# Kernel tuning notes

Hardware: AMD Instinct MI355X
Metric: run time of the kernel (lower is better)

The kernel has to match this reference:

```python
import jax, jax.numpy as jnp
import numpy as np

BANDWIDTH = 8.0  # gaussian kernel std


def setup_inputs() -> dict:
    key = jax.random.key(0)
    k1, k2 = jax.random.split(key)
    B, N, M, D = 2, 8192, 8192, 64
    return {
        "points": jax.random.normal(k1, (B, N, D), dtype=jnp.float32),
        "ref_points": jax.random.normal(k2, (B, M, D), dtype=jnp.float32),
    }


def reference(points, ref_points):
    # Squared pairwise distances via the |x|^2 + |y|^2 - 2<x,y> expansion
    # (same math as ((x_i - y_j)**2).sum(-1), avoids a [B,N,M,D] intermediate).
    sq_p = jnp.sum(points * points, axis=-1)          # [B,N]
    sq_r = jnp.sum(ref_points * ref_points, axis=-1)  # [B,M]
    s_ij = (sq_p[:, :, None] + sq_r[:, None, :]
            - 2.0 * jnp.einsum('bnd,bmd->bnm', points, ref_points))  # [B,N,M]
    # Gaussian kernel
    k_ij = jnp.exp(s_ij * (-1.0 / (2.0 * BANDWIDTH ** 2)))  # [B,N,M]
    # Weighted mean of reference points (nominator.sum(2) / k_ij.sum(2))
    nominator = jnp.einsum('bnm,bmd->bnd', k_ij, ref_points)  # [B,N,D]
    denominator = jnp.sum(k_ij, axis=-1, keepdims=True)       # [B,N,1]
    return nominator / denominator
```

## Files before the change

### kernel.cpp

```cpp
#include <hip/hip_runtime.h>

constexpr int B_ = 2, N_ = 8192, M_ = 8192, Dd = 64;
constexpr int TN = 128;
constexpr int TM = 64;
constexpr int SPLIT = 8;
constexpr int MCHUNK = M_ / SPLIT;
constexpr int NCHUNKS = MCHUNK / TM;
constexpr int NT = N_ / TN;
constexpr float LOG2E   = 1.4426950408889634f;
constexpr float SCALE_S = LOG2E / 64.0f;
constexpr float SCALE_N = -LOG2E / 128.0f;

using s16x8 = __attribute__((ext_vector_type(8))) short;
using f32x4 = __attribute__((ext_vector_type(4))) float;
using f32x2v = __attribute__((ext_vector_type(2))) float;
using bf16x2 = __attribute__((ext_vector_type(2))) __bf16;

#if defined(__has_builtin)
#if __has_builtin(__builtin_amdgcn_exp2f)
#define EXP2(x) __builtin_amdgcn_exp2f(x)
#endif
#endif
#ifndef EXP2
#define EXP2(x) exp2f(x)
#endif

__device__ __forceinline__ unsigned pk2(float lo, float hi) {
  f32x2v f;
  f[0] = lo;
  f[1] = hi;
  bf16x2 h = __builtin_convertvector(f, bf16x2);
  return __builtin_bit_cast(unsigned, h);
}
__device__ __forceinline__ f32x4 mfma16(s16x8 a, s16x8 b, f32x4 c) {
  return __builtin_amdgcn_mfma_f32_16x16x32_bf16(a, b, c, 0, 0, 0);
}


__global__ __launch_bounds__(256, 4) void msflash_kernel(
    const float* __restrict__ pts, const float* __restrict__ ref,
    float* __restrict__ num_acc, float* __restrict__ den_acc) {
  __shared__ unsigned short ldsY [TM][72];
  __shared__ unsigned short ldsYT[Dd][64];
  __shared__ unsigned short ldsP [4][32][72];
  __shared__ float lds_an2[TN];
  __shared__ float lds_bm2[TM];

  const int tid  = threadIdx.x;
  const int w    = tid >> 6;
  const int lane = tid & 63;
  const int l15  = lane & 15, quad = lane >> 4;
  const int ytsw = quad + (l15 & 7);

  const int s  = blockIdx.x & (SPLIT - 1);
  const int r  = blockIdx.x >> 3;
  const int bb = r / NT;
  const int nt = r % NT;
  const int n0 = nt * TN;
  const int m_begin = s * MCHUNK;

  unsigned short (*ldsX)[72] = (unsigned short (*)[72]) & ldsP[0][0][0];
  {
    const int rowl = tid >> 1, half = tid & 1;
    const float* gp = pts + ((size_t)bb * N_ + n0 + rowl) * Dd + half * 32;
    float sq = 0.f;
    unsigned pkd[16];
#pragma unroll
    for (int i = 0; i < 8; i++) {
      float4 f = ((const float4*)gp)[i];
      sq += f.x * f.x + f.y * f.y + f.z * f.z + f.w * f.w;
      pkd[2 * i + 0] = pk2(f.x, f.y);
      pkd[2 * i + 1] = pk2(f.z, f.w);
    }
    sq += __shfl_xor(sq, 1);
    if (half == 0) lds_an2[rowl] = sq * SCALE_N;
    uint4* dv = (uint4*)&ldsX[rowl][half * 32];
#pragma unroll
    for (int i = 0; i < 4; i++)
      dv[i] = make_uint4(pkd[4 * i], pkd[4 * i + 1], pkd[4 * i + 2], pkd[4 * i + 3]);
  }
  __syncthreads();

  s16x8 bx[2][2];
  float anr_s[2];
#pragma unroll
  for (int rt = 0; rt < 2; rt++) {
#pragma unroll
    for (int ks = 0; ks < 2; ks++)
      bx[rt][ks] = *(const s16x8*)&ldsX[w * 32 + rt * 16 + l15][ks * 32 + quad * 8];
    anr_s[rt] = lds_an2[w * 32 + rt * 16 + l15];
  }

  f32x4 o[2][4], den[2];
#pragma unroll
  for (int rt = 0; rt < 2; rt++) {
    den[rt] = f32x4{0.f, 0.f, 0.f, 0.f};
#pragma unroll
    for (int dt = 0; dt < 4; dt++) o[rt][dt] = f32x4{0.f, 0.f, 0.f, 0.f};
  }
  s16x8 ones;
#pragma unroll
  for (int j = 0; j < 8; j++) ones[j] = (l15 == 0) ? (short)0x3F80 : (short)0;

  for (int c = 0; c < NCHUNKS; c++) {
    __syncthreads();
    {
      const int rowl = tid >> 2, q = tid & 3;
      const float* gp = ref + ((size_t)bb * M_ + m_begin + c * TM + rowl) * Dd + q * 16;
      float sq = 0.f;
      unsigned pkd[8];
#pragma unroll
      for (int i = 0; i < 4; i++) {
        float4 f = ((const float4*)gp)[i];
        sq += f.x * f.x + f.y * f.y + f.z * f.z + f.w * f.w;
        pkd[2 * i + 0] = pk2(f.x, f.y);
        pkd[2 * i + 1] = pk2(f.z, f.w);
      }
      sq += __shfl_xor(sq, 1);
      sq += __shfl_xor(sq, 2);
      if (q == 0) lds_bm2[rowl] = sq * SCALE_N;
      uint4* dv = (uint4*)&ldsY[rowl][q * 16];
      dv[0] = make_uint4(pkd[0], pkd[1], pkd[2], pkd[3]);
      dv[1] = make_uint4(pkd[4], pkd[5], pkd[6], pkd[7]);
      const int tsw = (rowl >> 3) + 2 * q;
      const int mlo = rowl & 7;
#pragma unroll
      for (int j = 0; j < 8; j++) {
        const int d0 = q * 16 + 2 * j;
        const int c0 = (tsw + ((2 * j) & 7)) & 7;
        const int c1 = (tsw + ((2 * j + 1) & 7)) & 7;
        ldsYT[d0][(c0 << 3) + mlo]     = (unsigned short)pkd[j];
        ldsYT[d0 + 1][(c1 << 3) + mlo] = (unsigned short)(pkd[j] >> 16);
      }
    }
    __syncthreads();

    f32x4 sf[2][4];
#pragma unroll
    for (int ct = 0; ct < 4; ct++) {
      s16x8 a0 = *(const s16x8*)&ldsY[ct * 16 + l15][quad * 8];
      s16x8 a1 = *(const s16x8*)&ldsY[ct * 16 + l15][32 + quad * 8];
#pragma unroll
      for (int rt = 0; rt < 2; rt++) {
        f32x4 acc = f32x4{0.f, 0.f, 0.f, 0.f};
        acc = mfma16(a0, bx[rt][0], acc);
        acc = mfma16(a1, bx[rt][1], acc);
        sf[rt][ct] = acc;
      }
    }
#pragma unroll
    for (int ct = 0; ct < 4; ct++) {
      f32x4 bm = *(const f32x4*)&lds_bm2[ct * 16 + quad * 4];
#pragma unroll
      for (int rt = 0; rt < 2; rt++) {
        float e0 = EXP2(sf[rt][ct][0] * SCALE_S + (anr_s[rt] + bm[0]));
        float e1 = EXP2(sf[rt][ct][1] * SCALE_S + (anr_s[rt] + bm[1]));
        float e2 = EXP2(sf[rt][ct][2] * SCALE_S + (anr_s[rt] + bm[2]));
        float e3 = EXP2(sf[rt][ct][3] * SCALE_S + (anr_s[rt] + bm[3]));
        uint2 w2 = make_uint2(pk2(e0, e1), pk2(e2, e3));
        *(uint2*)&ldsP[w][rt * 16 + l15][ct * 16 + quad * 4] = w2;
      }
    }
    s16x8 pf[2][2];
#pragma unroll
    for (int rt = 0; rt < 2; rt++)
#pragma unroll
      for (int ks = 0; ks < 2; ks++)
        pf[rt][ks] = *(const s16x8*)&ldsP[w][rt * 16 + l15][ks * 32 + quad * 8];
#pragma unroll
    for (int dt = 0; dt < 4; dt++) {
      const unsigned short* yt = &ldsYT[dt * 16 + l15][0];
      s16x8 a0 = *(const s16x8*)&yt[(((ytsw + 2 * dt) & 7)) << 3];
      s16x8 a1 = *(const s16x8*)&yt[(((ytsw + 4 + 2 * dt) & 7)) << 3];
#pragma unroll
      for (int rt = 0; rt < 2; rt++) {
        o[rt][dt] = mfma16(a0, pf[rt][0], o[rt][dt]);
        o[rt][dt] = mfma16(a1, pf[rt][1], o[rt][dt]);
      }
    }
#pragma unroll
    for (int rt = 0; rt < 2; rt++) {
      den[rt] = mfma16(ones, pf[rt][0], den[rt]);
      den[rt] = mfma16(ones, pf[rt][1], den[rt]);
    }
  }

  float* ldsO = (float*)&ldsP[w][0][0];
  float* nb = num_acc + ((size_t)bb * N_ + n0) * Dd;
#pragma unroll
  for (int rt = 0; rt < 2; rt++) {
#pragma unroll
    for (int dt = 0; dt < 4; dt++) {
      const int base = l15 * 66 + dt * 16 + quad * 4;
      *(float2*)&ldsO[base + 0] = make_float2(o[rt][dt][0], o[rt][dt][1]);
      *(float2*)&ldsO[base + 2] = make_float2(o[rt][dt][2], o[rt][dt][3]);
    }
    const int nrow = w * 32 + rt * 16;
#pragma unroll
    for (int rr = 0; rr < 16; rr++) {
      float v = ldsO[rr * 66 + lane];
      atomicAdd(&nb[(size_t)(nrow + rr) * Dd + lane], v);
    }
    if (quad == 0)
      atomicAdd(&den_acc[(size_t)bb * N_ + n0 + nrow + l15], den[rt][0]);
  }
}

__global__ __launch_bounds__(256) void msdiv_kernel(
    const float* __restrict__ num, const float* __restrict__ den,
    float* __restrict__ out) {
  const int i = blockIdx.x * 256 + threadIdx.x;
  float4 v = ((const float4*)num)[i];
  const float inv = 1.0f / den[i >> 4];
  ((float4*)out)[i] = make_float4(v.x * inv, v.y * inv, v.z * inv, v.w * inv);
}

extern "C" void kernel_launch(void* const* d_in, const int* in_sizes, int n_in,
                              void* d_out, int out_size, void* d_ws, size_t ws_size,
                              hipStream_t stream) {
  const float* pts = (const float*)d_in[0];
  const float* ref = (const float*)d_in[1];
  float* out = (float*)d_out;
  float* num = (float*)d_ws;
  float* den = num + (size_t)B_ * N_ * Dd;
  const size_t acc_bytes = ((size_t)B_ * N_ * Dd + (size_t)B_ * N_) * sizeof(float);

  hipMemsetAsync(d_ws, 0, acc_bytes, stream);
  msflash_kernel<<<dim3(B_ * NT * SPLIT), dim3(256), 0, stream>>>(pts, ref, num, den);
  const int tot4 = B_ * N_ * Dd / 4;
  msdiv_kernel<<<dim3(tot4 / 256), dim3(256), 0, stream>>>(num, den, out);
}
```

Before: 129.3 us.

## Repartition S computation by ref rows per wave and register-prefetch ref tiles

Each wave now computes scores for its own 16 reference rows against all 128 query rows, keeping all query fragments in registers. It loads its ref rows straight from global into MFMA operand registers, so the row-major ldsY buffer goes away. The next chunk's ref data is prefetched into registers while the current chunk computes, which overlaps global load latency. The cost is higher register pressure (launch bounds lowered from 4 to 3 waves), a shared P buffer that every wave must exchange through, and a new transposed-layout swizzle.

```diff
diff --git a/kernel.cpp b/kernel.cpp
--- a/kernel.cpp
+++ b/kernel.cpp
@@ -35,14 +35,16 @@
 __device__ __forceinline__ f32x4 mfma16(s16x8 a, s16x8 b, f32x4 c) {
   return __builtin_amdgcn_mfma_f32_16x16x32_bf16(a, b, c, 0, 0, 0);
 }
-
-
-__global__ __launch_bounds__(256, 4) void msflash_kernel(
+__device__ __forceinline__ float dot4(float4 f) {
+  return f.x * f.x + f.y * f.y + f.z * f.z + f.w * f.w;
+}
+
+
+__global__ __launch_bounds__(256, 3) void msflash_kernel(
     const float* __restrict__ pts, const float* __restrict__ ref,
     float* __restrict__ num_acc, float* __restrict__ den_acc) {
-  __shared__ unsigned short ldsY [TM][72];
   __shared__ unsigned short ldsYT[Dd][64];
-  __shared__ unsigned short ldsP [4][32][72];
+  __shared__ unsigned short ldsP [128][72];
   __shared__ float lds_an2[TN];
   __shared__ float lds_bm2[TM];
 
@@ -50,16 +52,26 @@
   const int w    = tid >> 6;
   const int lane = tid & 63;
   const int l15  = lane & 15, quad = lane >> 4;
-  const int ytsw = quad + (l15 & 7);
 
   const int s  = blockIdx.x & (SPLIT - 1);
   const int r  = blockIdx.x >> 3;
   const int bb = r / NT;
-  const int nt = r % NT;
-  const int n0 = nt * TN;
+  const int nt_ = r % NT;
+  const int n0 = nt_ * TN;
   const int m_begin = s * MCHUNK;
 
-  unsigned short (*ldsX)[72] = (unsigned short (*)[72]) & ldsP[0][0][0];
+  const int wbase = (w * 2 + (l15 >> 3)) + 2 * quad;
+  const int mlo   = l15 & 7;
+  const int ytr   = quad + 2 * (l15 >> 3) + (l15 & 7);
+
+  const int myrow = w * 16 + l15;
+  const float* ybase = ref + ((size_t)bb * M_ + m_begin + myrow) * Dd + quad * 8;
+  float4 fv0 = ((const float4*)ybase)[0];
+  float4 fv1 = ((const float4*)ybase)[1];
+  float4 fv2 = ((const float4*)(ybase + 32))[0];
+  float4 fv3 = ((const float4*)(ybase + 32))[1];
+
+  unsigned short (*ldsX)[72] = (unsigned short (*)[72]) & ldsP[0][0];
   {
     const int rowl = tid >> 1, half = tid & 1;
     const float* gp = pts + ((size_t)bb * N_ + n0 + rowl) * Dd + half * 32;
@@ -68,7 +80,7 @@
 #pragma unroll
     for (int i = 0; i < 8; i++) {
       float4 f = ((const float4*)gp)[i];
-      sq += f.x * f.x + f.y * f.y + f.z * f.z + f.w * f.w;
+      sq += dot4(f);
       pkd[2 * i + 0] = pk2(f.x, f.y);
       pkd[2 * i + 1] = pk2(f.z, f.w);
     }
@@ -81,14 +93,14 @@
   }
   __syncthreads();
 
-  s16x8 bx[2][2];
-  float anr_s[2];
-#pragma unroll
-  for (int rt = 0; rt < 2; rt++) {
+  s16x8 bx[8][2];
+  float anr[8];
+#pragma unroll
+  for (int nt = 0; nt < 8; nt++) {
 #pragma unroll
     for (int ks = 0; ks < 2; ks++)
-      bx[rt][ks] = *(const s16x8*)&ldsX[w * 32 + rt * 16 + l15][ks * 32 + quad * 8];
-    anr_s[rt] = lds_an2[w * 32 + rt * 16 + l15];
+      bx[nt][ks] = *(const s16x8*)&ldsX[nt * 16 + l15][ks * 32 + quad * 8];
+    anr[nt] = lds_an2[nt * 16 + l15];
   }
 
   f32x4 o[2][4], den[2];
@@ -104,74 +116,62 @@
 
   for (int c = 0; c < NCHUNKS; c++) {
     __syncthreads();
-    {
-      const int rowl = tid >> 2, q = tid & 3;
-      const float* gp = ref + ((size_t)bb * M_ + m_begin + c * TM + rowl) * Dd + q * 16;
-      float sq = 0.f;
-      unsigned pkd[8];
-#pragma unroll
-      for (int i = 0; i < 4; i++) {
-        float4 f = ((const float4*)gp)[i];
-        sq += f.x * f.x + f.y * f.y + f.z * f.z + f.w * f.w;
-        pkd[2 * i + 0] = pk2(f.x, f.y);
-        pkd[2 * i + 1] = pk2(f.z, f.w);
-      }
-      sq += __shfl_xor(sq, 1);
-      sq += __shfl_xor(sq, 2);
-      if (q == 0) lds_bm2[rowl] = sq * SCALE_N;
-      uint4* dv = (uint4*)&ldsY[rowl][q * 16];
-      dv[0] = make_uint4(pkd[0], pkd[1], pkd[2], pkd[3]);
-      dv[1] = make_uint4(pkd[4], pkd[5], pkd[6], pkd[7]);
-      const int tsw = (rowl >> 3) + 2 * q;
-      const int mlo = rowl & 7;
-#pragma unroll
-      for (int j = 0; j < 8; j++) {
-        const int d0 = q * 16 + 2 * j;
-        const int c0 = (tsw + ((2 * j) & 7)) & 7;
-        const int c1 = (tsw + ((2 * j + 1) & 7)) & 7;
-        ldsYT[d0][(c0 << 3) + mlo]     = (unsigned short)pkd[j];
-        ldsYT[d0 + 1][(c1 << 3) + mlo] = (unsigned short)(pkd[j] >> 16);
-      }
+
+    unsigned pkA[4] = {pk2(fv0.x, fv0.y), pk2(fv0.z, fv0.w),
+                       pk2(fv1.x, fv1.y), pk2(fv1.z, fv1.w)};
+    unsigned pkB[4] = {pk2(fv2.x, fv2.y), pk2(fv2.z, fv2.w),
+                       pk2(fv3.x, fv3.y), pk2(fv3.z, fv3.w)};
+    float sq = dot4(fv0) + dot4(fv1) + dot4(fv2) + dot4(fv3);
+    sq += __shfl_xor(sq, 16);
+    sq += __shfl_xor(sq, 32);
+    if (quad == 0) lds_bm2[w * 16 + l15] = sq * SCALE_N;
+#pragma unroll
+    for (int j = 0; j < 4; j++) {
+      const int d0 = quad * 8 + 2 * j;
+      const int c0 = (wbase + 2 * j) & 7;
+      const int c1 = (wbase + 2 * j + 1) & 7;
+      ldsYT[d0     ][(c0 << 3) + mlo] = (unsigned short)pkA[j];
+      ldsYT[d0 + 1 ][(c1 << 3) + mlo] = (unsigned short)(pkA[j] >> 16);
+      ldsYT[d0 + 32][(c0 << 3) + mlo] = (unsigned short)pkB[j];
+      ldsYT[d0 + 33][(c1 << 3) + mlo] = (unsigned short)(pkB[j] >> 16);
+    }
+    s16x8 ay0 = __builtin_bit_cast(s16x8, make_uint4(pkA[0], pkA[1], pkA[2], pkA[3]));
+    s16x8 ay1 = __builtin_bit_cast(s16x8, make_uint4(pkB[0], pkB[1], pkB[2], pkB[3]));
+    const f32x4 bmv = *(const f32x4*)&lds_bm2[w * 16 + quad * 4];
+
+    if (c + 1 < NCHUNKS) {
+      const float* yp = ybase + (size_t)(c + 1) * TM * Dd;
+      fv0 = ((const float4*)yp)[0];
+      fv1 = ((const float4*)yp)[1];
+      fv2 = ((const float4*)(yp + 32))[0];
+      fv3 = ((const float4*)(yp + 32))[1];
+    }
+
+#pragma unroll
+    for (int nt = 0; nt < 8; nt++) {
+      f32x4 acc = f32x4{0.f, 0.f, 0.f, 0.f};
+      acc = mfma16(ay0, bx[nt][0], acc);
+      acc = mfma16(ay1, bx[nt][1], acc);
+      float e0 = EXP2(acc[0] * SCALE_S + (anr[nt] + bmv[0]));
+      float e1 = EXP2(acc[1] * SCALE_S + (anr[nt] + bmv[1]));
+      float e2 = EXP2(acc[2] * SCALE_S + (anr[nt] + bmv[2]));
+      float e3 = EXP2(acc[3] * SCALE_S + (anr[nt] + bmv[3]));
+      *(uint2*)&ldsP[nt * 16 + l15][w * 16 + quad * 4] =
+          make_uint2(pk2(e0, e1), pk2(e2, e3));
     }
     __syncthreads();
 
-    f32x4 sf[2][4];
-#pragma unroll
-    for (int ct = 0; ct < 4; ct++) {
-      s16x8 a0 = *(const s16x8*)&ldsY[ct * 16 + l15][quad * 8];
-      s16x8 a1 = *(const s16x8*)&ldsY[ct * 16 + l15][32 + quad * 8];
-#pragma unroll
-      for (int rt = 0; rt < 2; rt++) {
-        f32x4 acc = f32x4{0.f, 0.f, 0.f, 0.f};
-        acc = mfma16(a0, bx[rt][0], acc);
-        acc = mfma16(a1, bx[rt][1], acc);
-        sf[rt][ct] = acc;
-      }
-    }
-#pragma unroll
-    for (int ct = 0; ct < 4; ct++) {
-      f32x4 bm = *(const f32x4*)&lds_bm2[ct * 16 + quad * 4];
-#pragma unroll
-      for (int rt = 0; rt < 2; rt++) {
-        float e0 = EXP2(sf[rt][ct][0] * SCALE_S + (anr_s[rt] + bm[0]));
-        float e1 = EXP2(sf[rt][ct][1] * SCALE_S + (anr_s[rt] + bm[1]));
-        float e2 = EXP2(sf[rt][ct][2] * SCALE_S + (anr_s[rt] + bm[2]));
-        float e3 = EXP2(sf[rt][ct][3] * SCALE_S + (anr_s[rt] + bm[3]));
-        uint2 w2 = make_uint2(pk2(e0, e1), pk2(e2, e3));
-        *(uint2*)&ldsP[w][rt * 16 + l15][ct * 16 + quad * 4] = w2;
-      }
-    }
     s16x8 pf[2][2];
 #pragma unroll
     for (int rt = 0; rt < 2; rt++)
 #pragma unroll
       for (int ks = 0; ks < 2; ks++)
-        pf[rt][ks] = *(const s16x8*)&ldsP[w][rt * 16 + l15][ks * 32 + quad * 8];
+        pf[rt][ks] = *(const s16x8*)&ldsP[w * 32 + rt * 16 + l15][ks * 32 + quad * 8];
 #pragma unroll
     for (int dt = 0; dt < 4; dt++) {
       const unsigned short* yt = &ldsYT[dt * 16 + l15][0];
-      s16x8 a0 = *(const s16x8*)&yt[(((ytsw + 2 * dt) & 7)) << 3];
-      s16x8 a1 = *(const s16x8*)&yt[(((ytsw + 4 + 2 * dt) & 7)) << 3];
+      s16x8 a0 = *(const s16x8*)&yt[(((ytr + 4 * dt) & 7)) << 3];
+      s16x8 a1 = *(const s16x8*)&yt[(((ytr + 4 + 4 * dt) & 7)) << 3];
 #pragma unroll
       for (int rt = 0; rt < 2; rt++) {
         o[rt][dt] = mfma16(a0, pf[rt][0], o[rt][dt]);
@@ -185,7 +185,7 @@
     }
   }
 
-  float* ldsO = (float*)&ldsP[w][0][0];
+  float* ldsO = (float*)&ldsP[w * 32][0];
   float* nb = num_acc + ((size_t)bb * N_ + n0) * Dd;
 #pragma unroll
   for (int rt = 0; rt < 2; rt++) {
```

Result: slower. 148.8 us (+15.0%).

## Double-buffer reference tiles with register prefetch and swizzle P tile in LDS

Applied to the files above, without the earlier changes.

Reference tiles are now double-buffered in LDS. The next chunk's global loads are issued into registers a full iteration ahead, so only one barrier per chunk is needed instead of two. The P staging buffer gets an XOR-style swizzle in place of the padded layout to avoid bank conflicts. The larger shared-memory footprint lowers launch_bounds occupancy from 4 to 3 blocks per CU, trading occupancy for latency hiding.

```diff
diff --git a/kernel.cpp b/kernel.cpp
--- a/kernel.cpp
+++ b/kernel.cpp
@@ -35,31 +35,71 @@
 __device__ __forceinline__ f32x4 mfma16(s16x8 a, s16x8 b, f32x4 c) {
   return __builtin_amdgcn_mfma_f32_16x16x32_bf16(a, b, c, 0, 0, 0);
 }
-
-
-__global__ __launch_bounds__(256, 4) void msflash_kernel(
+__device__ __forceinline__ float dot4(float4 f) {
+  return f.x * f.x + f.y * f.y + f.z * f.z + f.w * f.w;
+}
+
+
+__global__ __launch_bounds__(256, 3) void msflash_kernel(
     const float* __restrict__ pts, const float* __restrict__ ref,
     float* __restrict__ num_acc, float* __restrict__ den_acc) {
-  __shared__ unsigned short ldsY [TM][72];
-  __shared__ unsigned short ldsYT[Dd][64];
-  __shared__ unsigned short ldsP [4][32][72];
+  __shared__ unsigned short ldsY2[2][TM][72];
+  __shared__ unsigned short ldsYT2[2][Dd][64];
+  __shared__ unsigned short ldsPp[4][32][64];
   __shared__ float lds_an2[TN];
-  __shared__ float lds_bm2[TM];
+  __shared__ float lds_bm2[2][TM];
 
   const int tid  = threadIdx.x;
   const int w    = tid >> 6;
   const int lane = tid & 63;
   const int l15  = lane & 15, quad = lane >> 4;
   const int ytsw = quad + (l15 & 7);
+  const int psw  = l15 & 7;
 
   const int s  = blockIdx.x & (SPLIT - 1);
   const int r  = blockIdx.x >> 3;
   const int bb = r / NT;
-  const int nt = r % NT;
-  const int n0 = nt * TN;
+  const int nt_ = r % NT;
+  const int n0 = nt_ * TN;
   const int m_begin = s * MCHUNK;
 
-  unsigned short (*ldsX)[72] = (unsigned short (*)[72]) & ldsP[0][0][0];
+  const int rowl_s = tid >> 2, q_s = tid & 3;
+  const float* ybase = ref + ((size_t)bb * M_ + m_begin + rowl_s) * Dd + q_s * 16;
+  float4 fv0, fv1, fv2, fv3;
+
+  auto loadfv = [&](int cc) {
+    const float* yp = ybase + (size_t)cc * TM * Dd;
+    fv0 = ((const float4*)yp)[0];
+    fv1 = ((const float4*)yp)[1];
+    fv2 = ((const float4*)yp)[2];
+    fv3 = ((const float4*)yp)[3];
+  };
+  auto stage = [&](int bp) {
+    unsigned pkd[8] = {pk2(fv0.x, fv0.y), pk2(fv0.z, fv0.w),
+                       pk2(fv1.x, fv1.y), pk2(fv1.z, fv1.w),
+                       pk2(fv2.x, fv2.y), pk2(fv2.z, fv2.w),
+                       pk2(fv3.x, fv3.y), pk2(fv3.z, fv3.w)};
+    float sq = dot4(fv0) + dot4(fv1) + dot4(fv2) + dot4(fv3);
+    sq += __shfl_xor(sq, 1);
+    sq += __shfl_xor(sq, 2);
+    if (q_s == 0) lds_bm2[bp][rowl_s] = sq * SCALE_N;
+    uint4* dv = (uint4*)&ldsY2[bp][rowl_s][q_s * 16];
+    dv[0] = make_uint4(pkd[0], pkd[1], pkd[2], pkd[3]);
+    dv[1] = make_uint4(pkd[4], pkd[5], pkd[6], pkd[7]);
+    const int tsw = (rowl_s >> 3) + 2 * q_s;
+    const int mlo = rowl_s & 7;
+#pragma unroll
+    for (int j = 0; j < 8; j++) {
+      const int d0 = q_s * 16 + 2 * j;
+      const int c0 = (tsw + ((2 * j) & 7)) & 7;
+      const int c1 = (tsw + ((2 * j + 1) & 7)) & 7;
+      ldsYT2[bp][d0][(c0 << 3) + mlo]     = (unsigned short)pkd[j];
+      ldsYT2[bp][d0 + 1][(c1 << 3) + mlo] = (unsigned short)(pkd[j] >> 16);
+    }
+  };
+
+  loadfv(0);
+  unsigned short (*ldsX)[72] = (unsigned short (*)[72]) & ldsY2[0][0][0];
   {
     const int rowl = tid >> 1, half = tid & 1;
     const float* gp = pts + ((size_t)bb * N_ + n0 + rowl) * Dd + half * 32;
@@ -68,7 +108,7 @@
 #pragma unroll
     for (int i = 0; i < 8; i++) {
       float4 f = ((const float4*)gp)[i];
-      sq += f.x * f.x + f.y * f.y + f.z * f.z + f.w * f.w;
+      sq += dot4(f);
       pkd[2 * i + 0] = pk2(f.x, f.y);
       pkd[2 * i + 1] = pk2(f.z, f.w);
     }
@@ -90,6 +130,11 @@
       bx[rt][ks] = *(const s16x8*)&ldsX[w * 32 + rt * 16 + l15][ks * 32 + quad * 8];
     anr_s[rt] = lds_an2[w * 32 + rt * 16 + l15];
   }
+  __syncthreads();
+
+  stage(0);
+  loadfv(1);
+  __syncthreads();
 
   f32x4 o[2][4], den[2];
 #pragma unroll
@@ -102,44 +147,13 @@
 #pragma unroll
   for (int j = 0; j < 8; j++) ones[j] = (l15 == 0) ? (short)0x3F80 : (short)0;
 
-  for (int c = 0; c < NCHUNKS; c++) {
-    __syncthreads();
-    {
-      const int rowl = tid >> 2, q = tid & 3;
-      const float* gp = ref + ((size_t)bb * M_ + m_begin + c * TM + rowl) * Dd + q * 16;
-      float sq = 0.f;
-      unsigned pkd[8];
-#pragma unroll
-      for (int i = 0; i < 4; i++) {
-        float4 f = ((const float4*)gp)[i];
-        sq += f.x * f.x + f.y * f.y + f.z * f.z + f.w * f.w;
-        pkd[2 * i + 0] = pk2(f.x, f.y);
-        pkd[2 * i + 1] = pk2(f.z, f.w);
-      }
-      sq += __shfl_xor(sq, 1);
-      sq += __shfl_xor(sq, 2);
-      if (q == 0) lds_bm2[rowl] = sq * SCALE_N;
-      uint4* dv = (uint4*)&ldsY[rowl][q * 16];
-      dv[0] = make_uint4(pkd[0], pkd[1], pkd[2], pkd[3]);
-      dv[1] = make_uint4(pkd[4], pkd[5], pkd[6], pkd[7]);
-      const int tsw = (rowl >> 3) + 2 * q;
-      const int mlo = rowl & 7;
-#pragma unroll
-      for (int j = 0; j < 8; j++) {
-        const int d0 = q * 16 + 2 * j;
-        const int c0 = (tsw + ((2 * j) & 7)) & 7;
-        const int c1 = (tsw + ((2 * j + 1) & 7)) & 7;
-        ldsYT[d0][(c0 << 3) + mlo]     = (unsigned short)pkd[j];
-        ldsYT[d0 + 1][(c1 << 3) + mlo] = (unsigned short)(pkd[j] >> 16);
-      }
-    }
-    __syncthreads();
-
+  int p = 0;
+  for (int c = 0; c < NCHUNKS; ++c) {
     f32x4 sf[2][4];
 #pragma unroll
     for (int ct = 0; ct < 4; ct++) {
-      s16x8 a0 = *(const s16x8*)&ldsY[ct * 16 + l15][quad * 8];
-      s16x8 a1 = *(const s16x8*)&ldsY[ct * 16 + l15][32 + quad * 8];
+      s16x8 a0 = *(const s16x8*)&ldsY2[p][ct * 16 + l15][quad * 8];
+      s16x8 a1 = *(const s16x8*)&ldsY2[p][ct * 16 + l15][32 + quad * 8];
 #pragma unroll
       for (int rt = 0; rt < 2; rt++) {
         f32x4 acc = f32x4{0.f, 0.f, 0.f, 0.f};
@@ -150,28 +164,31 @@
     }
 #pragma unroll
     for (int ct = 0; ct < 4; ct++) {
-      f32x4 bm = *(const f32x4*)&lds_bm2[ct * 16 + quad * 4];
+      f32x4 bm = *(const f32x4*)&lds_bm2[p][ct * 16 + quad * 4];
 #pragma unroll
       for (int rt = 0; rt < 2; rt++) {
         float e0 = EXP2(sf[rt][ct][0] * SCALE_S + (anr_s[rt] + bm[0]));
         float e1 = EXP2(sf[rt][ct][1] * SCALE_S + (anr_s[rt] + bm[1]));
         float e2 = EXP2(sf[rt][ct][2] * SCALE_S + (anr_s[rt] + bm[2]));
         float e3 = EXP2(sf[rt][ct][3] * SCALE_S + (anr_s[rt] + bm[3]));
-        uint2 w2 = make_uint2(pk2(e0, e1), pk2(e2, e3));
-        *(uint2*)&ldsP[w][rt * 16 + l15][ct * 16 + quad * 4] = w2;
+        const int oW = (2 * ct + (quad >> 1) + psw) & 7;
+        *(uint2*)&ldsPp[w][rt * 16 + l15][(oW << 3) + (quad & 1) * 4] =
+            make_uint2(pk2(e0, e1), pk2(e2, e3));
       }
     }
     s16x8 pf[2][2];
 #pragma unroll
     for (int rt = 0; rt < 2; rt++)
 #pragma unroll
-      for (int ks = 0; ks < 2; ks++)
-        pf[rt][ks] = *(const s16x8*)&ldsP[w][rt * 16 + l15][ks * 32 + quad * 8];
+      for (int ks = 0; ks < 2; ks++) {
+        const int oR = (4 * ks + quad + psw) & 7;
+        pf[rt][ks] = *(const s16x8*)&ldsPp[w][rt * 16 + l15][oR << 3];
+      }
 #pragma unroll
     for (int dt = 0; dt < 4; dt++) {
-      const unsigned short* yt = &ldsYT[dt * 16 + l15][0];
-      s16x8 a0 = *(const s16x8*)&yt[(((ytsw + 2 * dt) & 7)) << 3];
-      s16x8 a1 = *(const s16x8*)&yt[(((ytsw + 4 + 2 * dt) & 7)) << 3];
+      const unsigned short* yt = &ldsYT2[p][dt * 16 + l15][0];
+      s16x8 a0 = *(const s16x8*)&yt[((ytsw + 2 * dt) & 7) << 3];
+      s16x8 a1 = *(const s16x8*)&yt[((ytsw + 4 + 2 * dt) & 7) << 3];
 #pragma unroll
       for (int rt = 0; rt < 2; rt++) {
         o[rt][dt] = mfma16(a0, pf[rt][0], o[rt][dt]);
@@ -183,9 +200,13 @@
       den[rt] = mfma16(ones, pf[rt][0], den[rt]);
       den[rt] = mfma16(ones, pf[rt][1], den[rt]);
     }
-  }
-
-  float* ldsO = (float*)&ldsP[w][0][0];
+    stage(p ^ 1);
+    loadfv(c + 2 < NCHUNKS ? c + 2 : NCHUNKS - 1);
+    __syncthreads();
+    p ^= 1;
+  }
+
+  float* ldsO = (float*)&ldsY2[0][0][0] + (size_t)w * 1152;
   float* nb = num_acc + ((size_t)bb * N_ + n0) * Dd;
 #pragma unroll
   for (int rt = 0; rt < 2; rt++) {
```

Result: no change. 127.9 us (-1.1%).
